# Optimization experiments

Hardware: AMD Instinct MI355X
Metric: run time of the kernel (lower is better)

The kernel has to match this reference:

```python
import jax, jax.numpy as jnp
import numpy as np

N_NODES = 100000
N_EDGES = 3200000
IN_DIM = 8
HID = 64
N_LAYERS = 3
LN_EPS = 1e-5


def setup_inputs() -> dict:
    key = jax.random.key(0)
    ks = jax.random.split(key, 10)
    x = jax.random.normal(ks[0], (N_NODES, IN_DIM), dtype=jnp.float32)
    edge_src = jax.random.randint(ks[1], (N_EDGES,), 0, N_NODES, dtype=jnp.int32)
    edge_dst = jax.random.randint(ks[2], (N_EDGES,), 0, N_NODES, dtype=jnp.int32)
    # parameters
    W_in = jax.random.normal(ks[3], (HID, IN_DIM), dtype=jnp.float32) * 0.1
    b_in = jnp.zeros((HID,), dtype=jnp.float32)
    Ws_self = jax.random.normal(ks[4], (N_LAYERS, HID, HID), dtype=jnp.float32) * 0.1
    Ws_neigh = jax.random.normal(ks[5], (N_LAYERS, HID, HID), dtype=jnp.float32) * 0.1
    biases = jnp.zeros((N_LAYERS, HID), dtype=jnp.float32)
    gammas = jnp.ones((N_LAYERS, HID), dtype=jnp.float32)
    betas = jnp.zeros((N_LAYERS, HID), dtype=jnp.float32)
    return {"x": x, "edge_src": edge_src, "edge_dst": edge_dst,
            "W_in": W_in, "b_in": b_in, "Ws_self": Ws_self,
            "Ws_neigh": Ws_neigh, "biases": biases,
            "gammas": gammas, "betas": betas}


def _layer_norm(h, gamma, beta):
    mu = jnp.mean(h, axis=-1, keepdims=True)
    var = jnp.mean((h - mu) ** 2, axis=-1, keepdims=True)
    return (h - mu) * jax.lax.rsqrt(var + LN_EPS) * gamma + beta


def reference(x, edge_src, edge_dst, W_in, b_in, Ws_self, Ws_neigh, biases, gammas, betas):
    n = x.shape[0]
    # deg[v] = number of neighbors gathered for node v (edges ending at v)
    deg = jax.ops.segment_sum(jnp.ones_like(edge_dst, dtype=jnp.float32), edge_dst,
                              num_segments=n)  # (n,)
    inv_deg = jnp.where(deg > 0, 1.0 / jnp.maximum(deg, 1.0), 0.0)[:, None]

    h = jax.nn.relu(x @ W_in.T + b_in)  # (n, HID); dropout is identity in eval
    for l in range(N_LAYERS):
        # mean neighbor features: gather + scatter-add + normalize
        neigh_sum = jax.ops.segment_sum(h[edge_src], edge_dst, num_segments=n)
        neigh_mean = neigh_sum * inv_deg  # zero rows where deg==0, as in original
        h_self = h @ Ws_self[l].T
        h_neigh = neigh_mean @ Ws_neigh[l].T  # linear has no bias -> 0 when deg==0
        h_l = _layer_norm(h_self + h_neigh + biases[l], gammas[l], betas[l])
        h = h + jax.nn.relu(h_l)  # residual from DrBCEncoder
    return h
```

## Files before the change

### kernel.cpp

```cpp
#include <hip/hip_runtime.h>

#define HID 64
#define BSHIFT 9
#define NPB 512
#define P3TILE 4096
#define HISTB 512
#define PREPB 96

typedef unsigned int uint;
typedef unsigned short ushort;
typedef unsigned char uchar;
typedef float f32x2 __attribute__((ext_vector_type(2)));
typedef float f32x4 __attribute__((ext_vector_type(4)));
typedef short bf16x8 __attribute__((ext_vector_type(8)));

__device__ inline ushort f2b(float f) {
    uint u = __float_as_uint(f);
    return (ushort)((u + 0x7fffu + ((u >> 16) & 1u)) >> 16);
}

__device__ inline float b2f(ushort b) { return __uint_as_float((uint)b << 16); }

__device__ inline void accf8(f32x2* a, uint4 hv) {
    a[0] += __builtin_bit_cast(f32x2, __builtin_amdgcn_cvt_pk_f32_fp8(hv.x, false));
    a[1] += __builtin_bit_cast(f32x2, __builtin_amdgcn_cvt_pk_f32_fp8(hv.x, true));
    a[2] += __builtin_bit_cast(f32x2, __builtin_amdgcn_cvt_pk_f32_fp8(hv.y, false));
    a[3] += __builtin_bit_cast(f32x2, __builtin_amdgcn_cvt_pk_f32_fp8(hv.y, true));
    a[4] += __builtin_bit_cast(f32x2, __builtin_amdgcn_cvt_pk_f32_fp8(hv.z, false));
    a[5] += __builtin_bit_cast(f32x2, __builtin_amdgcn_cvt_pk_f32_fp8(hv.z, true));
    a[6] += __builtin_bit_cast(f32x2, __builtin_amdgcn_cvt_pk_f32_fp8(hv.w, false));
    a[7] += __builtin_bit_cast(f32x2, __builtin_amdgcn_cvt_pk_f32_fp8(hv.w, true));
}

__device__ inline uchar f2fp8(float f) {
    return (uchar)(__builtin_amdgcn_cvt_pk_fp8_f32(f, f, 0, false) & 0xff);
}


__global__ __launch_bounds__(256) void hist_input(const int* __restrict__ dst,
                                                  int* __restrict__ bcnt, int e, int nb,
                                                  const float* __restrict__ x,
                                                  const float* __restrict__ W_in,
                                                  const float* __restrict__ b_in,
                                                  ushort* __restrict__ hb,
                                                  uchar* __restrict__ h8, int n,
                                                  int inb,
                                                  const float* __restrict__ Ws,
                                                  const float* __restrict__ Wn,
                                                  ushort* __restrict__ Wcat) {
    __shared__ float smem[576];
    int t = threadIdx.x;
    int b = blockIdx.x;
    if (b < HISTB) {
        int* lh = (int*)smem;
        lh[t] = 0;
        __syncthreads();
        for (int i = b * 256 + t; i < e; i += HISTB * 256)
            atomicAdd(&lh[dst[i] >> BSHIFT], 1);
        __syncthreads();
        if (t < nb && lh[t]) atomicAdd(&bcnt[t], lh[t]);
        return;
    }
    if (b >= HISTB + inb) {
        int i = (b - HISTB - inb) * 256 + t;
        if (i < 3 * 8192) {
            int l = i >> 13;
            int r = i & 8191;
            int j = r >> 7;
            int k = r & 127;
            float v = (k < 64) ? Ws[l * 4096 + j * 64 + k]
                               : Wn[l * 4096 + j * 64 + (k - 64)];
            Wcat[i] = f2b(v);
        }
        return;
    }
    int ib = b - HISTB;
    float* WlT = smem;
    float* bl = smem + 512;
    for (int i = t; i < 512; i += 256) {
        int j = i >> 3, k = i & 7;
        WlT[k * 64 + j] = W_in[i];
    }
    if (t < 64) bl[t] = b_in[t];
    __syncthreads();
    int total2 = n * 32;
    for (int i = ib * 256 + t; i < total2; i += inb * 256) {
        int v = i >> 5;
        int jp = i & 31;
        int j0 = jp * 2, j1 = jp * 2 + 1;
        const float* xr = x + (size_t)v * 8;
        float s0 = bl[j0], s1 = bl[j1];
#pragma unroll
        for (int k = 0; k < 8; ++k) {
            float xv = xr[k];
            s0 += xv * WlT[k * 64 + j0];
            s1 += xv * WlT[k * 64 + j1];
        }
        float o0 = fmaxf(s0, 0.0f), o1 = fmaxf(s1, 0.0f);
        ((uint*)hb)[i] = (uint)f2b(o0) | ((uint)f2b(o1) << 16);
        int pk = __builtin_amdgcn_cvt_pk_fp8_f32(o0, o1, 0, false);
        *(ushort*)&h8[(size_t)2 * i] = (ushort)(pk & 0xffff);
    }
}

__global__ void bucket_scan(const int* __restrict__ bcnt, int* __restrict__ bbase,
                            int* __restrict__ bcur, int* __restrict__ offsets,
                            int e, int nb, int n) {
    __shared__ int sd[256];
    int t = threadIdx.x;
    int v = (t < nb) ? bcnt[t] : 0;
    sd[t] = v;
    __syncthreads();
    for (int off = 1; off < 256; off <<= 1) {
        int u = (t >= off) ? sd[t - off] : 0;
        __syncthreads();
        sd[t] += u;
        __syncthreads();
    }
    int excl = t ? sd[t - 1] : 0;
    if (t < nb) { bbase[t] = excl; bcur[t] = excl; }
    if (t == nb) bbase[t] = e;
    if (t == 0) offsets[n] = e;
}

__global__ __launch_bounds__(256) void partition(const int* __restrict__ src,
                                                 const int* __restrict__ dst,
                                                 int* __restrict__ bcur,
                                                 int* __restrict__ pair, int e, int nb) {
    __shared__ int lh[256], cb[256];
    int t = threadIdx.x;
    int base = blockIdx.x * P3TILE;
    lh[t] = 0;
    __syncthreads();
    int s[16], d[16], r[16];
    if (base + P3TILE <= e) {
        const int4* s4 = (const int4*)(src + base);
        const int4* d4 = (const int4*)(dst + base);
#pragma unroll
        for (int k = 0; k < 4; ++k) {
            int4 sv = s4[t * 4 + k];
            int4 dv = d4[t * 4 + k];
            s[k * 4 + 0] = sv.x; s[k * 4 + 1] = sv.y;
            s[k * 4 + 2] = sv.z; s[k * 4 + 3] = sv.w;
            d[k * 4 + 0] = dv.x; d[k * 4 + 1] = dv.y;
            d[k * 4 + 2] = dv.z; d[k * 4 + 3] = dv.w;
        }
#pragma unroll
        for (int k = 0; k < 16; ++k)
            r[k] = atomicAdd(&lh[d[k] >> BSHIFT], 1);
        __syncthreads();
        if (t < nb && lh[t]) cb[t] = atomicAdd(&bcur[t], lh[t]);
        __syncthreads();
#pragma unroll
        for (int k = 0; k < 16; ++k)
            pair[cb[d[k] >> BSHIFT] + r[k]] = (s[k] << BSHIFT) | (d[k] & (NPB - 1));
    } else {
#pragma unroll
        for (int k = 0; k < 16; ++k) {
            int i = base + t * 16 + k;
            if (i < e) {
                s[k] = src[i];
                d[k] = dst[i];
                r[k] = atomicAdd(&lh[d[k] >> BSHIFT], 1);
            }
        }
        __syncthreads();
        if (t < nb && lh[t]) cb[t] = atomicAdd(&bcur[t], lh[t]);
        __syncthreads();
#pragma unroll
        for (int k = 0; k < 16; ++k) {
            int i = base + t * 16 + k;
            if (i < e)
                pair[cb[d[k] >> BSHIFT] + r[k]] = (s[k] << BSHIFT) | (d[k] & (NPB - 1));
        }
    }
}

__global__ __launch_bounds__(1024) void build_csr(const int* __restrict__ pair,
                                                  const int* __restrict__ bbase,
                                                  int* __restrict__ offsets,
                                                  float* __restrict__ invdeg,
                                                  int* __restrict__ col, int n) {
    __shared__ int bins[NPB], cur[NPB], sd[NPB];
    int b = blockIdx.x, t = threadIdx.x;
    int cbase = bbase[b], cend = bbase[b + 1];
    int v0 = b << BSHIFT;
    if (t < NPB) bins[t] = 0;
    __syncthreads();
    for (int i = cbase + t; i < cend; i += 1024)
        atomicAdd(&bins[pair[i] & (NPB - 1)], 1);
    __syncthreads();
    int d = (t < NPB) ? bins[t] : 0;
    if (t < NPB) sd[t] = d;
    __syncthreads();
    for (int off = 1; off < NPB; off <<= 1) {
        int u = (t < NPB && t >= off) ? sd[t - off] : 0;
        __syncthreads();
        if (t < NPB) sd[t] += u;
        __syncthreads();
    }
    if (t < NPB) {
        int excl = sd[t] - d;
        cur[t] = excl;
        int v = v0 + t;
        if (v < n) {
            offsets[v] = cbase + excl;
            invdeg[v] = d > 0 ? 1.0f / (float)d : 0.0f;
        }
    }
    __syncthreads();
    for (int i = cbase + t; i < cend; i += 1024) {
        int p = pair[i];
        int pos = atomicAdd(&cur[p & (NPB - 1)], 1);
        col[cbase + pos] = p >> BSHIFT;
    }
}


template <int LAST>
__global__ __launch_bounds__(256) void agg_tf(
    const uchar* __restrict__ h8in, const ushort* __restrict__ hbm,
    ushort* __restrict__ hbout, uchar* __restrict__ h8out,
    float* __restrict__ outF,
    const int* __restrict__ offsets, const int* __restrict__ col,
    const float* __restrict__ invdeg,
    const ushort* __restrict__ Wcat, const float* __restrict__ bias,
    const float* __restrict__ gamma, const float* __restrict__ beta, int n) {
    __shared__ ushort nmlds[4][16][72];
    int t = threadIdx.x, lane = t & 63, wid = t >> 6;
    int ntiles = (n + 15) >> 4;
    int tile = blockIdx.x * 4 + wid;
    if (tile >= ntiles) return;
    int m0 = tile << 4;
    int q = lane >> 4;
    int fl = lane & 15;
    int e4 = lane & 3;
    int sl = (lane >> 2) & 3;
    for (int p = 0; p < 4; ++p) {
        int v = m0 + p * 4 + q;
        int vv = v < n ? v : n - 1;
        int o0 = offsets[vv], o1 = offsets[vv + 1];
        int deg = o1 - o0;
        const int* cp = col + o0;
        int deg16 = deg & ~15;
        f32x2 acc2[8];
        float* af = (float*)acc2;
#pragma unroll
        for (int k = 0; k < 8; ++k) acc2[k] = f32x2{0.f, 0.f};
        for (int base = 0; base < deg16; base += 16) {
            int idx16 = cp[base + fl];
#pragma unroll
            for (int jj = 0; jj < 16; jj += 4) {
                int ne = __shfl(idx16, q * 16 + jj + sl);
                uint4 hv = *(const uint4*)&h8in[(size_t)ne * HID + e4 * 16];
                accf8(acc2, hv);
            }
        }
        for (int jj = 0; jj < 16; jj += 4) {
            if (deg16 + jj >= deg) break;
            int j = deg16 + jj + sl;
            if (j < deg) {
                int ne = cp[j];
                uint4 hv = *(const uint4*)&h8in[(size_t)ne * HID + e4 * 16];
                accf8(acc2, hv);
            }
        }
#pragma unroll
        for (int k = 0; k < 16; ++k) {
            af[k] += __shfl_xor(af[k], 4);
            af[k] += __shfl_xor(af[k], 8);
        }
        if (sl == 0) {
            float s = invdeg[vv];
            uint4 lo, hi;
            lo.x = (uint)f2b(af[0] * s) | ((uint)f2b(af[1] * s) << 16);
            lo.y = (uint)f2b(af[2] * s) | ((uint)f2b(af[3] * s) << 16);
            lo.z = (uint)f2b(af[4] * s) | ((uint)f2b(af[5] * s) << 16);
            lo.w = (uint)f2b(af[6] * s) | ((uint)f2b(af[7] * s) << 16);
            hi.x = (uint)f2b(af[8] * s) | ((uint)f2b(af[9] * s) << 16);
            hi.y = (uint)f2b(af[10] * s) | ((uint)f2b(af[11] * s) << 16);
            hi.z = (uint)f2b(af[12] * s) | ((uint)f2b(af[13] * s) << 16);
            hi.w = (uint)f2b(af[14] * s) | ((uint)f2b(af[15] * s) << 16);
            *(uint4*)&nmlds[wid][p * 4 + q][e4 * 16] = lo;
            *(uint4*)&nmlds[wid][p * 4 + q][e4 * 16 + 8] = hi;
        }
    }
    int c = lane & 15, g = lane >> 4;
    bf16x8 Bf[4][4];
#pragma unroll
    for (int tt = 0; tt < 4; ++tt)
#pragma unroll
        for (int s = 0; s < 4; ++s)
            Bf[s][tt] = *(const bf16x8*)&Wcat[(tt * 16 + c) * 128 + s * 32 + g * 8];
    float bcol[4], gcol[4], btc[4];
#pragma unroll
    for (int tt = 0; tt < 4; ++tt) {
        bcol[tt] = bias[tt * 16 + c];
        gcol[tt] = gamma[tt * 16 + c];
        btc[tt] = beta[tt * 16 + c];
    }
    int node = m0 + c;
    int nodeL = node < n ? node : n - 1;
    bf16x8 Af[4];
#pragma unroll
    for (int s = 0; s < 2; ++s)
        Af[s] = *(const bf16x8*)&hbm[(size_t)nodeL * HID + s * 32 + g * 8];
#pragma unroll
    for (int s = 0; s < 2; ++s)
        Af[2 + s] = *(const bf16x8*)&nmlds[wid][c][s * 32 + g * 8];
    f32x4 acc[4] = {{0, 0, 0, 0}, {0, 0, 0, 0}, {0, 0, 0, 0}, {0, 0, 0, 0}};
#pragma unroll
    for (int tt = 0; tt < 4; ++tt)
#pragma unroll
        for (int s = 0; s < 4; ++s)
            acc[tt] = __builtin_amdgcn_mfma_f32_16x16x32_bf16(Af[s], Bf[s][tt],
                                                             acc[tt], 0, 0, 0);
    float v[4][4];
#pragma unroll
    for (int tt = 0; tt < 4; ++tt)
#pragma unroll
        for (int r = 0; r < 4; ++r) v[tt][r] = acc[tt][r] + bcol[tt];
#pragma unroll
    for (int r = 0; r < 4; ++r) {
        float s = v[0][r] + v[1][r] + v[2][r] + v[3][r];
        s += __shfl_xor(s, 1);
        s += __shfl_xor(s, 2);
        s += __shfl_xor(s, 4);
        s += __shfl_xor(s, 8);
        float mu = s * (1.0f / 64.0f);
        float ss = 0.f;
#pragma unroll
        for (int tt = 0; tt < 4; ++tt) {
            float d = v[tt][r] - mu;
            ss += d * d;
        }
        ss += __shfl_xor(ss, 1);
        ss += __shfl_xor(ss, 2);
        ss += __shfl_xor(ss, 4);
        ss += __shfl_xor(ss, 8);
        float inv = rsqrtf(ss * (1.0f / 64.0f) + 1e-5f);
        int nr = m0 + g * 4 + r;
        if (nr < n) {
#pragma unroll
            for (int tt = 0; tt < 4; ++tt) {
                int j = tt * 16 + c;
                float hl = (v[tt][r] - mu) * inv * gcol[tt] + btc[tt];
                float hv = b2f(hbm[(size_t)nr * HID + j]);
                float o = hv + fmaxf(hl, 0.0f);
                if (LAST) {
                    outF[(size_t)nr * HID + j] = o;
                } else {
                    hbout[(size_t)nr * HID + j] = f2b(o);
                    h8out[(size_t)nr * HID + j] = f2fp8(o);
                }
            }
        }
    }
}


extern "C" void kernel_launch(void* const* d_in, const int* in_sizes, int n_in,
                              void* d_out, int out_size, void* d_ws, size_t ws_size,
                              hipStream_t stream) {
    const float* x = (const float*)d_in[0];
    const int* edge_src = (const int*)d_in[1];
    const int* edge_dst = (const int*)d_in[2];
    const float* W_in = (const float*)d_in[3];
    const float* b_in = (const float*)d_in[4];
    const float* Ws_self = (const float*)d_in[5];
    const float* Ws_neigh = (const float*)d_in[6];
    const float* biases = (const float*)d_in[7];
    const float* gammas = (const float*)d_in[8];
    const float* betas = (const float*)d_in[9];
    float* out = (float*)d_out;

    int n = in_sizes[0] / 8;
    int e = in_sizes[1];
    int nb = (n + NPB - 1) >> BSHIFT;

    char* w = (char*)d_ws;
    size_t off = 0;
    auto carve = [&](size_t bytes) -> void* {
        void* p = w + off;
        off = (off + bytes + 255) & ~(size_t)255;
        return p;
    };
    int* offsets = (int*)carve((size_t)(n + 1) * 4);
    float* invdeg = (float*)carve((size_t)n * 4);
    int* bcnt = (int*)carve(1024 * 4);
    int* bbase = (int*)carve(1024 * 4);
    int* bcur = (int*)carve(1024 * 4);
    int* col = (int*)carve((size_t)e * 4);
    int* pairbuf = (int*)carve((size_t)e * 4);
    ushort* hb = (ushort*)carve((size_t)n * HID * 2);
    uchar* h8A = (uchar*)carve((size_t)n * HID);
    uchar* h8B = (uchar*)carve((size_t)n * HID);
    ushort* Wcat = (ushort*)carve(3 * 64 * 128 * 2);
    (void)ws_size;

    hipMemsetAsync(bcnt, 0, 1024 * 4, stream);
    hist_input<<<HISTB + 2048 + PREPB, 256, 0, stream>>>(edge_dst, bcnt, e, nb,
                                                         x, W_in, b_in, hb, h8A, n,
                                                         2048, Ws_self, Ws_neigh, Wcat);
    bucket_scan<<<1, 256, 0, stream>>>(bcnt, bbase, bcur, offsets, e, nb, n);
    partition<<<(e + P3TILE - 1) / P3TILE, 256, 0, stream>>>(edge_src, edge_dst, bcur,
                                                            pairbuf, e, nb);
    build_csr<<<nb, 1024, 0, stream>>>(pairbuf, bbase, offsets, invdeg, col, n);

    int ntiles = (n + 15) >> 4;
    int ablocks = (ntiles + 3) / 4;
    uchar* hin = h8A;
    uchar* hout = h8B;
    for (int l = 0; l < 3; ++l) {
        if (l < 2) {
            agg_tf<0><<<ablocks, 256, 0, stream>>>(hin, hb, hb, hout, out,
                                                   offsets, col, invdeg,
                                                   Wcat + (size_t)l * 8192,
                                                   biases + l * 64, gammas + l * 64,
                                                   betas + l * 64, n);
        } else {
            agg_tf<1><<<ablocks, 256, 0, stream>>>(hin, hb, hb, hout, out,
                                                   offsets, col, invdeg,
                                                   Wcat + (size_t)l * 8192,
                                                   biases + l * 64, gammas + l * 64,
                                                   betas + l * 64, n);
        }
        uchar* tmp = hin; hin = hout; hout = tmp;
    }
}
```

Before: 289.0 us.

## Split each 16-node tile across four waves with shared-memory LayerNorm reduction

Before, each wave owned a 16-node tile, aggregated four nodes per pass over four passes, then computed all 64 output columns. Now a block owns one 16-node tile: each wave aggregates four nodes in a single pass and computes a 16-column slice of the GEMM. LayerNorm statistics are reduced across waves through shared memory using sum and sum-of-squares. The aim is to spread the gather latency across more waves and cut per-wave register use for weights, at the cost of two block barriers and a less stable one-pass variance formula.

```diff
diff --git a/kernel.cpp b/kernel.cpp
--- a/kernel.cpp
+++ b/kernel.cpp
@@ -226,18 +226,16 @@
     const float* __restrict__ invdeg,
     const ushort* __restrict__ Wcat, const float* __restrict__ bias,
     const float* __restrict__ gamma, const float* __restrict__ beta, int n) {
-    __shared__ ushort nmlds[4][16][72];
+    __shared__ ushort nmlds[16][72];
+    __shared__ float red[16][4][2];
     int t = threadIdx.x, lane = t & 63, wid = t >> 6;
-    int ntiles = (n + 15) >> 4;
-    int tile = blockIdx.x * 4 + wid;
-    if (tile >= ntiles) return;
-    int m0 = tile << 4;
+    int m0 = blockIdx.x << 4;
     int q = lane >> 4;
     int fl = lane & 15;
     int e4 = lane & 3;
     int sl = (lane >> 2) & 3;
-    for (int p = 0; p < 4; ++p) {
-        int v = m0 + p * 4 + q;
+    {
+        int v = m0 + wid * 4 + q;
         int vv = v < n ? v : n - 1;
         int o0 = offsets[vv], o1 = offsets[vv + 1];
         int deg = o1 - o0;
@@ -281,24 +279,19 @@
             hi.y = (uint)f2b(af[10] * s) | ((uint)f2b(af[11] * s) << 16);
             hi.z = (uint)f2b(af[12] * s) | ((uint)f2b(af[13] * s) << 16);
             hi.w = (uint)f2b(af[14] * s) | ((uint)f2b(af[15] * s) << 16);
-            *(uint4*)&nmlds[wid][p * 4 + q][e4 * 16] = lo;
-            *(uint4*)&nmlds[wid][p * 4 + q][e4 * 16 + 8] = hi;
-        }
-    }
+            int row = wid * 4 + q;
+            *(uint4*)&nmlds[row][e4 * 16] = lo;
+            *(uint4*)&nmlds[row][e4 * 16 + 8] = hi;
+        }
+    }
+    __syncthreads();
     int c = lane & 15, g = lane >> 4;
-    bf16x8 Bf[4][4];
-#pragma unroll
-    for (int tt = 0; tt < 4; ++tt)
-#pragma unroll
-        for (int s = 0; s < 4; ++s)
-            Bf[s][tt] = *(const bf16x8*)&Wcat[(tt * 16 + c) * 128 + s * 32 + g * 8];
-    float bcol[4], gcol[4], btc[4];
-#pragma unroll
-    for (int tt = 0; tt < 4; ++tt) {
-        bcol[tt] = bias[tt * 16 + c];
-        gcol[tt] = gamma[tt * 16 + c];
-        btc[tt] = beta[tt * 16 + c];
-    }
+    int jc = wid * 16 + c;
+    bf16x8 Bf[4];
+#pragma unroll
+    for (int s = 0; s < 4; ++s)
+        Bf[s] = *(const bf16x8*)&Wcat[jc * 128 + s * 32 + g * 8];
+    float bcol = bias[jc], gcol = gamma[jc], btc = beta[jc];
     int node = m0 + c;
     int nodeL = node < n ? node : n - 1;
     bf16x8 Af[4];
@@ -307,52 +300,46 @@
         Af[s] = *(const bf16x8*)&hbm[(size_t)nodeL * HID + s * 32 + g * 8];
 #pragma unroll
     for (int s = 0; s < 2; ++s)
-        Af[2 + s] = *(const bf16x8*)&nmlds[wid][c][s * 32 + g * 8];
-    f32x4 acc[4] = {{0, 0, 0, 0}, {0, 0, 0, 0}, {0, 0, 0, 0}, {0, 0, 0, 0}};
-#pragma unroll
-    for (int tt = 0; tt < 4; ++tt)
-#pragma unroll
-        for (int s = 0; s < 4; ++s)
-            acc[tt] = __builtin_amdgcn_mfma_f32_16x16x32_bf16(Af[s], Bf[s][tt],
-                                                             acc[tt], 0, 0, 0);
-    float v[4][4];
-#pragma unroll
-    for (int tt = 0; tt < 4; ++tt)
-#pragma unroll
-        for (int r = 0; r < 4; ++r) v[tt][r] = acc[tt][r] + bcol[tt];
+        Af[2 + s] = *(const bf16x8*)&nmlds[c][s * 32 + g * 8];
+    f32x4 acc = {0, 0, 0, 0};
+#pragma unroll
+    for (int s = 0; s < 4; ++s)
+        acc = __builtin_amdgcn_mfma_f32_16x16x32_bf16(Af[s], Bf[s], acc, 0, 0, 0);
+    float v4[4];
+#pragma unroll
+    for (int r = 0; r < 4; ++r) v4[r] = acc[r] + bcol;
 #pragma unroll
     for (int r = 0; r < 4; ++r) {
-        float s = v[0][r] + v[1][r] + v[2][r] + v[3][r];
-        s += __shfl_xor(s, 1);
-        s += __shfl_xor(s, 2);
-        s += __shfl_xor(s, 4);
-        s += __shfl_xor(s, 8);
-        float mu = s * (1.0f / 64.0f);
-        float ss = 0.f;
-#pragma unroll
-        for (int tt = 0; tt < 4; ++tt) {
-            float d = v[tt][r] - mu;
-            ss += d * d;
-        }
-        ss += __shfl_xor(ss, 1);
-        ss += __shfl_xor(ss, 2);
-        ss += __shfl_xor(ss, 4);
-        ss += __shfl_xor(ss, 8);
-        float inv = rsqrtf(ss * (1.0f / 64.0f) + 1e-5f);
-        int nr = m0 + g * 4 + r;
+        float s1 = v4[r];
+        float s2 = v4[r] * v4[r];
+        s1 += __shfl_xor(s1, 1); s2 += __shfl_xor(s2, 1);
+        s1 += __shfl_xor(s1, 2); s2 += __shfl_xor(s2, 2);
+        s1 += __shfl_xor(s1, 4); s2 += __shfl_xor(s2, 4);
+        s1 += __shfl_xor(s1, 8); s2 += __shfl_xor(s2, 8);
+        if (c == 0) {
+            red[g * 4 + r][wid][0] = s1;
+            red[g * 4 + r][wid][1] = s2;
+        }
+    }
+    __syncthreads();
+#pragma unroll
+    for (int r = 0; r < 4; ++r) {
+        int row = g * 4 + r;
+        float s1 = red[row][0][0] + red[row][1][0] + red[row][2][0] + red[row][3][0];
+        float s2 = red[row][0][1] + red[row][1][1] + red[row][2][1] + red[row][3][1];
+        float mu = s1 * (1.0f / 64.0f);
+        float var = fmaxf(s2 * (1.0f / 64.0f) - mu * mu, 0.0f);
+        float inv = rsqrtf(var + 1e-5f);
+        int nr = m0 + row;
         if (nr < n) {
-#pragma unroll
-            for (int tt = 0; tt < 4; ++tt) {
-                int j = tt * 16 + c;
-                float hl = (v[tt][r] - mu) * inv * gcol[tt] + btc[tt];
-                float hv = b2f(hbm[(size_t)nr * HID + j]);
-                float o = hv + fmaxf(hl, 0.0f);
-                if (LAST) {
-                    outF[(size_t)nr * HID + j] = o;
-                } else {
-                    hbout[(size_t)nr * HID + j] = f2b(o);
-                    h8out[(size_t)nr * HID + j] = f2fp8(o);
-                }
+            float hl = (v4[r] - mu) * inv * gcol + btc;
+            float hv = b2f(hbm[(size_t)nr * HID + jc]);
+            float o = hv + fmaxf(hl, 0.0f);
+            if (LAST) {
+                outF[(size_t)nr * HID + jc] = o;
+            } else {
+                hbout[(size_t)nr * HID + jc] = f2b(o);
+                h8out[(size_t)nr * HID + jc] = f2fp8(o);
             }
         }
     }
@@ -408,22 +395,21 @@
     build_csr<<<nb, 1024, 0, stream>>>(pairbuf, bbase, offsets, invdeg, col, n);
 
     int ntiles = (n + 15) >> 4;
-    int ablocks = (ntiles + 3) / 4;
     uchar* hin = h8A;
     uchar* hout = h8B;
     for (int l = 0; l < 3; ++l) {
         if (l < 2) {
-            agg_tf<0><<<ablocks, 256, 0, stream>>>(hin, hb, hb, hout, out,
-                                                   offsets, col, invdeg,
-                                                   Wcat + (size_t)l * 8192,
-                                                   biases + l * 64, gammas + l * 64,
-                                                   betas + l * 64, n);
+            agg_tf<0><<<ntiles, 256, 0, stream>>>(hin, hb, hb, hout, out,
+                                                  offsets, col, invdeg,
+                                                  Wcat + (size_t)l * 8192,
+                                                  biases + l * 64, gammas + l * 64,
+                                                  betas + l * 64, n);
         } else {
-            agg_tf<1><<<ablocks, 256, 0, stream>>>(hin, hb, hb, hout, out,
-                                                   offsets, col, invdeg,
-                                                   Wcat + (size_t)l * 8192,
-                                                   biases + l * 64, gammas + l * 64,
-                                                   betas + l * 64, n);
+            agg_tf<1><<<ntiles, 256, 0, stream>>>(hin, hb, hb, hout, out,
+                                                  offsets, col, invdeg,
+                                                  Wcat + (size_t)l * 8192,
+                                                  biases + l * 64, gammas + l * 64,
+                                                  betas + l * 64, n);
         }
         uchar* tmp = hin; hin = hout; hout = tmp;
     }
```

Result: slower. 314.0 us (+8.6%).
